# Kernel optimization log

Hardware: AMD Instinct MI355X
Metric: run time of the kernel (lower is better)

## Reference

```python
import jax, jax.numpy as jnp
import numpy as np

B, D, H, W, C = 8, 24, 24, 24, 192
NH = 6
WS = (4, 4, 4)
SS = (2, 2, 2)
HIDDEN = 4 * C
CPB_H = 512


def _buffers():
    wd, wh, ww = WS
    rd = np.arange(-(wd - 1), wd, dtype=np.float32)
    rh = np.arange(-(wh - 1), wh, dtype=np.float32)
    rw = np.arange(-(ww - 1), ww, dtype=np.float32)
    table = np.stack(np.meshgrid(rd, rh, rw, indexing='ij'), axis=-1)[None]  # (1,2wd-1,2wh-1,2ww-1,3)
    table[..., 0] /= (wd - 1)
    table[..., 1] /= (wh - 1)
    table[..., 2] /= (ww - 1)
    table *= 8.0
    table = np.sign(table) * np.log2(np.abs(table) + 1.0) / np.log2(8.0)
    coords = np.stack(np.meshgrid(np.arange(wd), np.arange(wh), np.arange(ww), indexing='ij'))
    cf = coords.reshape(3, -1)
    rel = (cf[:, :, None] - cf[:, None, :]).transpose(1, 2, 0).astype(np.int64)
    rel[..., 0] += wd - 1
    rel[..., 1] += wh - 1
    rel[..., 2] += ww - 1
    rel[..., 0] *= (2 * wh - 1) * (2 * ww - 1)
    rel[..., 1] *= (2 * ww - 1)
    return table.astype(np.float32), rel.sum(-1).astype(np.int32)


def _attn_mask():
    wd, wh, ww = WS
    img = np.zeros((1, D, H, W, 1), np.float32)
    cnt = 0
    def sl(w, s):
        return (slice(0, -w), slice(-w, -s), slice(-s, None))
    for d_ in sl(wd, SS[0]):
        for h_ in sl(wh, SS[1]):
            for w_ in sl(ww, SS[2]):
                img[:, d_, h_, w_, :] = cnt
                cnt += 1
    mw = img.reshape(1, D // wd, wd, H // wh, wh, W // ww, ww, 1)
    mw = mw.transpose(0, 1, 3, 5, 2, 4, 6, 7).reshape(-1, wd * wh * ww)  # (nW, N)
    am = mw[:, None, :] - mw[:, :, None]
    return np.where(am != 0, -100.0, 0.0).astype(np.float32)


def setup_inputs() -> dict:
    key = jax.random.key(0)
    ks = jax.random.split(key, 8)
    w = lambda k, shape: jax.random.normal(k, shape, jnp.float32) * 0.02
    table, rpi = _buffers()
    return {
        'x': jax.random.normal(ks[0], (B, D, H, W, C), jnp.float32),
        'norm1_w': jnp.ones((C,), jnp.float32), 'norm1_b': jnp.zeros((C,), jnp.float32),
        'qkv_w': w(ks[1], (3 * C, C)),
        'q_bias': jnp.zeros((C,), jnp.float32), 'v_bias': jnp.zeros((C,), jnp.float32),
        'logit_scale': jnp.log(10.0) * jnp.ones((NH, 1, 1), jnp.float32),
        'cpb_w1': w(ks[2], (CPB_H, 3)), 'cpb_b1': jnp.zeros((CPB_H,), jnp.float32),
        'cpb_w2': w(ks[3], (NH, CPB_H)),
        'proj_w': w(ks[4], (C, C)), 'proj_b': jnp.zeros((C,), jnp.float32),
        'norm2_w': jnp.ones((C,), jnp.float32), 'norm2_b': jnp.zeros((C,), jnp.float32),
        'fc1_w': w(ks[5], (HIDDEN, C)), 'fc1_b': jnp.zeros((HIDDEN,), jnp.float32),
        'fc2_w': w(ks[6], (C, HIDDEN)), 'fc2_b': jnp.zeros((C,), jnp.float32),
        'rel_table': jnp.asarray(table),
        'rel_index': jnp.asarray(rpi),
        'attn_mask': jnp.asarray(_attn_mask()),
    }


def _ln(x, w, b):
    mu = x.mean(-1, keepdims=True)
    var = ((x - mu) ** 2).mean(-1, keepdims=True)
    return (x - mu) * jax.lax.rsqrt(var + 1e-5) * w + b


def _forward(x, norm1_w, norm1_b, qkv_w, q_bias, v_bias, logit_scale,
             cpb_w1, cpb_b1, cpb_w2, proj_w, proj_b, norm2_w, norm2_b,
             fc1_w, fc1_b, fc2_w, fc2_b, rel_table, rel_index, attn_mask):
    wd, wh, ww = WS
    N = wd * wh * ww
    hd = C // NH
    shortcut = x
    h = _ln(x, norm1_w, norm1_b)
    h = jnp.roll(h, (-SS[0], -SS[1], -SS[2]), axis=(1, 2, 3))
    # window partition -> (B*nW, N, C)
    xw = h.reshape(B, D // wd, wd, H // wh, wh, W // ww, ww, C)
    xw = xw.transpose(0, 1, 3, 5, 2, 4, 6, 7).reshape(-1, N, C)
    B_ = xw.shape[0]
    # NOTE: faithful to torch source, where qkv is recomputed via self.qkv(x)
    # (bias=False), discarding the assembled qkv_bias. q_bias/v_bias thus unused.
    qkv = (xw @ qkv_w.T).reshape(B_, N, 3, NH, hd).transpose(2, 0, 3, 1, 4)
    q, k, v = qkv[0], qkv[1], qkv[2]  # each (B_, NH, N, hd)
    qn = q / jnp.maximum(jnp.linalg.norm(q, axis=-1, keepdims=True), 1e-12)
    kn = k / jnp.maximum(jnp.linalg.norm(k, axis=-1, keepdims=True), 1e-12)
    attn = jnp.einsum('bhnd,bhmd->bhnm', qn, kn)
    scale = jnp.exp(jnp.minimum(logit_scale, jnp.log(100.0)))  # (NH,1,1)
    attn = attn * scale
    # continuous position bias MLP -> gather per relative index
    bias_table = jax.nn.relu(rel_table.reshape(-1, 3) @ cpb_w1.T + cpb_b1) @ cpb_w2.T  # (T, NH)
    rpb = bias_table[rel_index.reshape(-1)].reshape(N, N, NH).transpose(2, 0, 1)
    attn = attn + 16.0 * jax.nn.sigmoid(rpb)[None]
    nW = attn_mask.shape[0]
    attn = attn.reshape(B_ // nW, nW, NH, N, N) + attn_mask[None, :, None]
    attn = jax.nn.softmax(attn.reshape(B_, NH, N, N), axis=-1)
    out = jnp.einsum('bhnm,bhmd->bhnd', attn, v).transpose(0, 2, 1, 3).reshape(B_, N, C)
    out = out @ proj_w.T + proj_b
    # window reverse -> (B, D, H, W, C)
    out = out.reshape(B, D // wd, H // wh, W // ww, wd, wh, ww, C)
    out = out.transpose(0, 1, 4, 2, 5, 3, 6, 7).reshape(B, D, H, W, C)
    out = jnp.roll(out, (SS[0], SS[1], SS[2]), axis=(1, 2, 3))
    h = shortcut + out
    m = _ln(h, norm2_w, norm2_b)
    m = jax.nn.gelu(m @ fc1_w.T + fc1_b, approximate=False)
    m = m @ fc2_w.T + fc2_b
    return h + m


def reference(x, norm1_w, norm1_b, qkv_w, q_bias, v_bias, logit_scale,
              cpb_w1, cpb_b1, cpb_w2, proj_w, proj_b, norm2_w, norm2_b,
              fc1_w, fc1_b, fc2_w, fc2_b, rel_table, rel_index, attn_mask):
    return _forward(x, norm1_w, norm1_b, qkv_w, q_bias, v_bias, logit_scale,
                    cpb_w1, cpb_b1, cpb_w2, proj_w, proj_b, norm2_w, norm2_b,
                    fc1_w, fc1_b, fc2_w, fc2_b, rel_table, rel_index, attn_mask)
```

## Files before the change

### kernel.cpp

```cpp
#include <hip/hip_runtime.h>
#include <hip/hip_bf16.h>
#include <math.h>

typedef __attribute__((ext_vector_type(8))) short bf16x8;
typedef __attribute__((ext_vector_type(4))) float f32x4;

__device__ inline ushort f2bf(float f) {
    __hip_bfloat16 h = __float2bfloat16(f);
    return *reinterpret_cast<ushort*>(&h);
}
__device__ inline float bf2f(ushort u) {
    return __uint_as_float(((unsigned int)u) << 16);
}

__global__ __launch_bounds__(256) void k_cpb_table(
        const float* __restrict__ rtab, const float* __restrict__ w1,
        const float* __restrict__ b1, const float* __restrict__ w2,
        float* __restrict__ table_out) {
    int idx = blockIdx.x * 256 + threadIdx.x;
    if (idx >= 343 * 6) return;
    int r = idx / 6, head = idx - r * 6;
    float t0 = rtab[r*3+0], t1 = rtab[r*3+1], t2 = rtab[r*3+2];
    float s = 0.f;
    for (int j = 0; j < 512; ++j) {
        float a = t0*w1[j*3+0] + t1*w1[j*3+1] + t2*w1[j*3+2] + b1[j];
        a = fmaxf(a, 0.f);
        s += a * w2[head*512 + j];
    }
    table_out[idx] = s;
}

__global__ __launch_bounds__(256) void k_bias16(
        const float* __restrict__ table_out, const int* __restrict__ ridx,
        float* __restrict__ bias16) {
    int idx = blockIdx.x * 256 + threadIdx.x;
    if (idx >= 6 * 64 * 64) return;
    int head = idx >> 12;
    int nm = idx & 4095;
    float v = table_out[ridx[nm] * 6 + head];
    bias16[idx] = 16.f / (1.f + expf(-v));
}

__global__ __launch_bounds__(256) void k_wcvt(
        const float* __restrict__ qkvw, const float* __restrict__ f1w,
        const float* __restrict__ f2w, const float* __restrict__ pw,
        ushort* __restrict__ Wqb, ushort* __restrict__ W1b,
        ushort* __restrict__ W2b, ushort* __restrict__ Wpb) {
    int i = blockIdx.x * 256 + threadIdx.x;
    W1b[i] = f2bf(f1w[i]);
    W2b[i] = f2bf(f2w[i]);
    if (i < 110592) Wqb[i] = f2bf(qkvw[i]);
    if (i < 36864)  Wpb[i] = f2bf(pw[i]);
}

__global__ __launch_bounds__(256) void k_ln1(
        const float* __restrict__ x, const float* __restrict__ nw,
        const float* __restrict__ nb, ushort* __restrict__ buf1) {
    const int wb = blockIdx.x;
    const int b = wb / 216, win = wb - b * 216;
    const int wdi = win / 36, whi = (win / 6) % 6, wwi = win % 6;
    const int t = threadIdx.x;
    const int n = t >> 2, sub = t & 3;
    const int id = n >> 4, ih = (n >> 2) & 3, iw = n & 3;
    const int dsrc = (wdi*4 + id + 2) % 24;
    const int hsrc = (whi*4 + ih + 2) % 24;
    const int wsrc = (wwi*4 + iw + 2) % 24;
    const float* xr = x + (size_t)(((b*24 + dsrc)*24 + hsrc)*24 + wsrc) * 192 + sub*48;
    float4 q[12];
    float sum = 0.f, ssum = 0.f;
    #pragma unroll
    for (int j = 0; j < 12; ++j) {
        q[j] = reinterpret_cast<const float4*>(xr)[j];
        sum  += q[j].x + q[j].y + q[j].z + q[j].w;
        ssum += q[j].x*q[j].x + q[j].y*q[j].y + q[j].z*q[j].z + q[j].w*q[j].w;
    }
    sum  += __shfl_xor(sum, 1);  sum  += __shfl_xor(sum, 2);
    ssum += __shfl_xor(ssum, 1); ssum += __shfl_xor(ssum, 2);
    float mu = sum * (1.f/192.f);
    float inv = rsqrtf(ssum * (1.f/192.f) - mu*mu + 1e-5f);
    ushort* op = buf1 + ((size_t)wb*64 + n)*192 + sub*48;
    #pragma unroll
    for (int j = 0; j < 12; ++j) {
        int c = sub*48 + j*4;
        ushort4 o;
        o.x = f2bf((q[j].x - mu)*inv*nw[c+0] + nb[c+0]);
        o.y = f2bf((q[j].y - mu)*inv*nw[c+1] + nb[c+1]);
        o.z = f2bf((q[j].z - mu)*inv*nw[c+2] + nb[c+2]);
        o.w = f2bf((q[j].w - mu)*inv*nw[c+3] + nb[c+3]);
        *reinterpret_cast<ushort4*>(op + j*4) = o;
    }
}

__global__ __launch_bounds__(256) void k_attn3(
        const ushort* __restrict__ buf1, const ushort* __restrict__ Wqb,
        const float* __restrict__ ls, const float* __restrict__ bias16,
        const float* __restrict__ amask, ushort* __restrict__ buf2) {
    __shared__ ushort QK[2][3][64][40];
    __shared__ ushort Vt[3][32][72];
    __shared__ ushort Pl[4][16][72];
    const int wb = blockIdx.x;
    const int win = wb % 216;
    const int t = threadIdx.x;
    const int wid = t >> 6, lane = t & 63;
    const int fr = lane & 15, fg = lane >> 4;
    const int trow = wid * 16;
    const ushort* Abase = buf1 + (size_t)wb * 12288 + (size_t)(trow + fr) * 192 + fg * 8;

    for (int g = 0; g < 2; ++g) {
        if (g) __syncthreads();
        f32x4 acc[18] = {};
        #pragma unroll
        for (int ks = 0; ks < 6; ++ks) {
            bf16x8 a = *(const bf16x8*)(Abase + ks*32);
            #pragma unroll
            for (int ct = 0; ct < 18; ++ct) {
                const int seg = ct / 6, u = ct % 6;
                const int gcol = seg*192 + g*96 + u*16;
                bf16x8 b = *(const bf16x8*)(Wqb + (size_t)(gcol + fr)*192 + ks*32 + fg*8);
                acc[ct] = __builtin_amdgcn_mfma_f32_16x16x32_bf16(a, b, acc[ct], 0, 0, 0);
            }
        }
        #pragma unroll
        for (int ct = 0; ct < 18; ++ct) {
            const int seg = ct / 6, u = ct % 6;
            const int hl = u >> 1, dp = u & 1;
            if (seg < 2) {
                #pragma unroll
                for (int e = 0; e < 4; ++e)
                    QK[seg][hl][trow + fg*4 + e][dp*16 + fr] = f2bf(acc[ct][e]);
            } else {
                ushort4 v4;
                v4.x = f2bf(acc[ct][0]); v4.y = f2bf(acc[ct][1]);
                v4.z = f2bf(acc[ct][2]); v4.w = f2bf(acc[ct][3]);
                *reinterpret_cast<ushort4*>(&Vt[hl][dp*16 + fr][trow + fg*4]) = v4;
            }
        }
        __syncthreads();
        {
            float scq[3];
            #pragma unroll
            for (int hl = 0; hl < 3; ++hl)
                scq[hl] = expf(fminf(ls[g*3 + hl], 4.6051701859880914f));
            for (int rr = t; rr < 384; rr += 256) {
                const int mat = rr / 192, rem = rr - mat*192;
                const int hl = rem >> 6, n = rem & 63;
                ushort* p = &QK[mat][hl][n][0];
                float vals[32];
                float ss = 0.f;
                #pragma unroll
                for (int j = 0; j < 8; ++j) {
                    ushort4 u4 = *reinterpret_cast<const ushort4*>(p + j*4);
                    float a0 = bf2f(u4.x), a1 = bf2f(u4.y), a2 = bf2f(u4.z), a3 = bf2f(u4.w);
                    vals[j*4+0]=a0; vals[j*4+1]=a1; vals[j*4+2]=a2; vals[j*4+3]=a3;
                    ss += a0*a0 + a1*a1 + a2*a2 + a3*a3;
                }
                float f = 1.f / fmaxf(sqrtf(ss), 1e-12f);
                if (mat == 0) f *= (hl == 0 ? scq[0] : (hl == 1 ? scq[1] : scq[2]));
                #pragma unroll
                for (int j = 0; j < 8; ++j) {
                    ushort4 o;
                    o.x = f2bf(vals[j*4+0]*f); o.y = f2bf(vals[j*4+1]*f);
                    o.z = f2bf(vals[j*4+2]*f); o.w = f2bf(vals[j*4+3]*f);
                    *reinterpret_cast<ushort4*>(p + j*4) = o;
                }
            }
        }
        __syncthreads();
        #pragma unroll 1
        for (int hl = 0; hl < 3; ++hl) {
            const int h = g*3 + hl;
            bf16x8 qf = *(const bf16x8*)&QK[0][hl][trow + fr][fg*8];
            f32x4 accS[4] = {};
            #pragma unroll
            for (int j = 0; j < 4; ++j) {
                bf16x8 kf = *(const bf16x8*)&QK[1][hl][j*16 + fr][fg*8];
                accS[j] = __builtin_amdgcn_mfma_f32_16x16x32_bf16(qf, kf, accS[j], 0, 0, 0);
            }
            float s[4][4];
            const float* bi = bias16 + h*4096;
            const float* mk = amask + (size_t)win*4096;
            #pragma unroll
            for (int e = 0; e < 4; ++e) {
                const int r = trow + fg*4 + e;
                #pragma unroll
                for (int j = 0; j < 4; ++j) {
                    const int c = j*16 + fr;
                    s[j][e] = accS[j][e] + bi[r*64 + c] + mk[r*64 + c];
                }
            }
            #pragma unroll
            for (int e = 0; e < 4; ++e) {
                float m0 = fmaxf(fmaxf(s[0][e], s[1][e]), fmaxf(s[2][e], s[3][e]));
                m0 = fmaxf(m0, __shfl_xor(m0, 1));
                m0 = fmaxf(m0, __shfl_xor(m0, 2));
                m0 = fmaxf(m0, __shfl_xor(m0, 4));
                m0 = fmaxf(m0, __shfl_xor(m0, 8));
                float s0 = 0.f;
                #pragma unroll
                for (int j = 0; j < 4; ++j) { s[j][e] = expf(s[j][e] - m0); s0 += s[j][e]; }
                s0 += __shfl_xor(s0, 1);
                s0 += __shfl_xor(s0, 2);
                s0 += __shfl_xor(s0, 4);
                s0 += __shfl_xor(s0, 8);
                const float rs = 1.f / s0;
                #pragma unroll
                for (int j = 0; j < 4; ++j)
                    Pl[wid][fg*4 + e][j*16 + fr] = f2bf(s[j][e] * rs);
            }
            f32x4 accO[2] = {};
            #pragma unroll
            for (int kk = 0; kk < 2; ++kk) {
                bf16x8 pa = *(const bf16x8*)&Pl[wid][fr][kk*32 + fg*8];
                #pragma unroll
                for (int j = 0; j < 2; ++j) {
                    bf16x8 vb = *(const bf16x8*)&Vt[hl][j*16 + fr][kk*32 + fg*8];
                    accO[j] = __builtin_amdgcn_mfma_f32_16x16x32_bf16(pa, vb, accO[j], 0, 0, 0);
                }
            }
            #pragma unroll
            for (int j = 0; j < 2; ++j) {
                #pragma unroll
                for (int e = 0; e < 4; ++e) {
                    buf2[(size_t)wb*12288 + (size_t)(trow + fg*4 + e)*192 + h*32 + j*16 + fr]
                        = f2bf(accO[j][e]);
                }
            }
        }
    }
}

__global__ __launch_bounds__(256) void k_proj(
        const ushort* __restrict__ buf2, const float* __restrict__ x,
        const ushort* __restrict__ Wpb, const float* __restrict__ pb,
        float* __restrict__ out) {
    __shared__ ushort As[64 * 200];
    __shared__ int rowbase[64];
    const int t = threadIdx.x;
    const size_t base = (size_t)blockIdx.x * 64;
    if (t < 64) {
        int dst = (int)base + t;
        int b = dst / 13824, r1 = dst - b * 13824;
        int d = r1 / 576, h2 = (r1 / 24) % 24, w2 = r1 % 24;
        int dd = (d + 22) % 24, hh = (h2 + 22) % 24, ww = (w2 + 22) % 24;
        int win = ((dd >> 2)*6 + (hh >> 2))*6 + (ww >> 2);
        int n = ((dd & 3) << 4) | ((hh & 3) << 2) | (ww & 3);
        rowbase[t] = ((b*216 + win)*64 + n) * 192;
    }
    __syncthreads();
    {
        const int r = t >> 2, q = t & 3;
        const ushort* src = buf2 + rowbase[r] + q*48;
        #pragma unroll
        for (int i = 0; i < 6; ++i)
            *(bf16x8*)(As + r*200 + q*48 + i*8) = *(const bf16x8*)(src + i*8);
    }
    __syncthreads();

    const int wid = t >> 6, lane = t & 63;
    const int fr = lane & 15, fg = lane >> 4;
    const int trow = wid * 16;
    f32x4 acc[12] = {};
    #pragma unroll
    for (int ks = 0; ks < 6; ++ks) {
        bf16x8 a = *(const bf16x8*)(As + (trow + fr)*200 + ks*32 + fg*8);
        #pragma unroll
        for (int j = 0; j < 12; ++j) {
            bf16x8 b = *(const bf16x8*)(Wpb + (size_t)(j*16 + fr)*192 + ks*32 + fg*8);
            acc[j] = __builtin_amdgcn_mfma_f32_16x16x32_bf16(a, b, acc[j], 0, 0, 0);
        }
    }
    #pragma unroll
    for (int j = 0; j < 12; ++j) {
        int c = j*16 + fr;
        float bias = pb[c];
        #pragma unroll
        for (int e = 0; e < 4; ++e) {
            size_t idx = (base + trow + fg*4 + e)*192 + c;
            out[idx] = x[idx] + acc[j][e] + bias;
        }
    }
}

__global__ __launch_bounds__(256) void k_mlp2(
        const ushort* __restrict__ W1b, const ushort* __restrict__ W2b,
        const float* __restrict__ n2w, const float* __restrict__ n2b,
        const float* __restrict__ f1b, const float* __restrict__ f2b,
        float* __restrict__ out) {
    __shared__ ushort As[64 * 200];
    __shared__ ushort Hs[64 * 136];
    const int t = threadIdx.x;
    const size_t tok0 = (size_t)blockIdx.x * 64;

    {
        const int r = t >> 2, q = t & 3;
        const float* hp = out + (tok0 + r) * 192 + q * 48;
        float4 v[12];
        float sum = 0.f, ssum = 0.f;
        #pragma unroll
        for (int j = 0; j < 12; ++j) {
            v[j] = reinterpret_cast<const float4*>(hp)[j];
            sum  += v[j].x + v[j].y + v[j].z + v[j].w;
            ssum += v[j].x*v[j].x + v[j].y*v[j].y + v[j].z*v[j].z + v[j].w*v[j].w;
        }
        sum  += __shfl_xor(sum, 1);  sum  += __shfl_xor(sum, 2);
        ssum += __shfl_xor(ssum, 1); ssum += __shfl_xor(ssum, 2);
        float mu = sum * (1.f/192.f);
        float inv = rsqrtf(ssum * (1.f/192.f) - mu*mu + 1e-5f);
        #pragma unroll
        for (int j = 0; j < 12; ++j) {
            int c = q*48 + j*4;
            ushort4 o;
            o.x = f2bf((v[j].x - mu)*inv*n2w[c+0] + n2b[c+0]);
            o.y = f2bf((v[j].y - mu)*inv*n2w[c+1] + n2b[c+1]);
            o.z = f2bf((v[j].z - mu)*inv*n2w[c+2] + n2b[c+2]);
            o.w = f2bf((v[j].w - mu)*inv*n2w[c+3] + n2b[c+3]);
            *reinterpret_cast<ushort4*>(As + r*200 + c) = o;
        }
    }
    __syncthreads();

    const int wid = t >> 6, lane = t & 63;
    const int fr = lane & 15, fg = lane >> 4;
    const int trow = wid * 16;
    f32x4 acc2[12] = {};

    for (int hb = 0; hb < 768; hb += 128) {
        f32x4 acc1[8] = {};
        #pragma unroll
        for (int ks = 0; ks < 6; ++ks) {
            bf16x8 a = *(const bf16x8*)(As + (trow + fr)*200 + ks*32 + fg*8);
            #pragma unroll
            for (int j = 0; j < 8; ++j) {
                bf16x8 b = *(const bf16x8*)(W1b + (size_t)(hb + j*16 + fr)*192 + ks*32 + fg*8);
                acc1[j] = __builtin_amdgcn_mfma_f32_16x16x32_bf16(a, b, acc1[j], 0, 0, 0);
            }
        }
        __syncthreads();
        #pragma unroll
        for (int j = 0; j < 8; ++j) {
            float bias = f1b[hb + j*16 + fr];
            #pragma unroll
            for (int e = 0; e < 4; ++e) {
                float h = acc1[j][e] + bias;
                h = 0.5f*h*(1.f + erff(h*0.70710678118654752f));
                Hs[(trow + fg*4 + e)*136 + j*16 + fr] = f2bf(h);
            }
        }
        __syncthreads();
        #pragma unroll
        for (int ks = 0; ks < 4; ++ks) {
            bf16x8 a = *(const bf16x8*)(Hs + (trow + fr)*136 + ks*32 + fg*8);
            #pragma unroll
            for (int j = 0; j < 12; ++j) {
                bf16x8 b = *(const bf16x8*)(W2b + (size_t)(j*16 + fr)*768 + hb + ks*32 + fg*8);
                acc2[j] = __builtin_amdgcn_mfma_f32_16x16x32_bf16(a, b, acc2[j], 0, 0, 0);
            }
        }
    }

    #pragma unroll
    for (int j = 0; j < 12; ++j) {
        int c = j*16 + fr;
        float bias = f2b[c];
        #pragma unroll
        for (int e = 0; e < 4; ++e) {
            size_t idx = (tok0 + trow + fg*4 + e)*192 + c;
            out[idx] += acc2[j][e] + bias;
        }
    }
}

extern "C" void kernel_launch(void* const* d_in, const int* in_sizes, int n_in,
                              void* d_out, int out_size, void* d_ws, size_t ws_size,
                              hipStream_t stream) {
    const float* x     = (const float*)d_in[0];
    const float* n1w   = (const float*)d_in[1];
    const float* n1b   = (const float*)d_in[2];
    const float* qkvw  = (const float*)d_in[3];
    const float* ls    = (const float*)d_in[6];
    const float* cpw1  = (const float*)d_in[7];
    const float* cpb1  = (const float*)d_in[8];
    const float* cpw2  = (const float*)d_in[9];
    const float* pw    = (const float*)d_in[10];
    const float* pb    = (const float*)d_in[11];
    const float* n2w   = (const float*)d_in[12];
    const float* n2b   = (const float*)d_in[13];
    const float* f1w   = (const float*)d_in[14];
    const float* f1b   = (const float*)d_in[15];
    const float* f2w   = (const float*)d_in[16];
    const float* f2b   = (const float*)d_in[17];
    const float* rtab  = (const float*)d_in[18];
    const int*   ridx  = (const int*)d_in[19];
    const float* amask = (const float*)d_in[20];
    float* out = (float*)d_out;

    ushort* buf1 = (ushort*)d_ws;
    ushort* buf2 = buf1 + 21233664;
    ushort* Wqb  = buf2 + 21233664;
    ushort* W1b  = Wqb + 110592;
    ushort* W2b  = W1b + 147456;
    ushort* Wpb  = W2b + 147456;
    float*  tblo = (float*)(Wpb + 36864);
    float*  b16  = tblo + 2064;

    k_cpb_table<<<dim3(9),    dim3(256), 0, stream>>>(rtab, cpw1, cpb1, cpw2, tblo);
    k_bias16   <<<dim3(96),   dim3(256), 0, stream>>>(tblo, ridx, b16);
    k_wcvt     <<<dim3(576),  dim3(256), 0, stream>>>(qkvw, f1w, f2w, pw, Wqb, W1b, W2b, Wpb);
    k_ln1      <<<dim3(1728), dim3(256), 0, stream>>>(x, n1w, n1b, buf1);
    k_attn3    <<<dim3(1728), dim3(256), 0, stream>>>(buf1, Wqb, ls, b16, amask, buf2);
    k_proj     <<<dim3(1728), dim3(256), 0, stream>>>(buf2, x, Wpb, pb, out);
    k_mlp2     <<<dim3(1728), dim3(256), 0, stream>>>(W1b, W2b, n2w, n2b, f1b, f2b, out);
}
```

Baseline: 1.150 ms.

## Give each wave 32 tokens in MLP kernel to reuse weight fragments

The MLP kernel now assigns 32 tokens per wave (128 per block) instead of 16, so every W1/W2 fragment loaded from global memory feeds two MFMAs. This halves weight traffic per token. LayerNorm output and the GELU hidden tile become per-wave private, which removes the block-wide __syncthreads. The A fragments are held in registers across the hidden loop, and the hidden chunk shrinks to 64. The risk is higher register pressure (acc2 grows to 24 f32x4 plus 12 A fragments) under launch_bounds(256,2), and the grid is halved.

```diff
diff --git a/kernel.cpp b/kernel.cpp
--- a/kernel.cpp
+++ b/kernel.cpp
@@ -281,79 +281,90 @@
     }
 }
 
-__global__ __launch_bounds__(256) void k_mlp2(
+__global__ __launch_bounds__(256, 2) void k_mlp3(
         const ushort* __restrict__ W1b, const ushort* __restrict__ W2b,
         const float* __restrict__ n2w, const float* __restrict__ n2b,
         const float* __restrict__ f1b, const float* __restrict__ f2b,
         float* __restrict__ out) {
-    __shared__ ushort As[64 * 200];
-    __shared__ ushort Hs[64 * 136];
+    __shared__ ushort As[4][32][200];
+    __shared__ ushort Hs[4][32][68];
     const int t = threadIdx.x;
-    const size_t tok0 = (size_t)blockIdx.x * 64;
+    const int wid = t >> 6, lane = t & 63;
+    const size_t tok0 = (size_t)blockIdx.x * 128 + wid * 32;
 
     {
-        const int r = t >> 2, q = t & 3;
-        const float* hp = out + (tok0 + r) * 192 + q * 48;
-        float4 v[12];
+        const int r = lane >> 1, half = lane & 1;
+        const float* hp = out + (tok0 + r) * 192 + half * 96;
+        float4 v[24];
         float sum = 0.f, ssum = 0.f;
         #pragma unroll
-        for (int j = 0; j < 12; ++j) {
+        for (int j = 0; j < 24; ++j) {
             v[j] = reinterpret_cast<const float4*>(hp)[j];
             sum  += v[j].x + v[j].y + v[j].z + v[j].w;
             ssum += v[j].x*v[j].x + v[j].y*v[j].y + v[j].z*v[j].z + v[j].w*v[j].w;
         }
-        sum  += __shfl_xor(sum, 1);  sum  += __shfl_xor(sum, 2);
-        ssum += __shfl_xor(ssum, 1); ssum += __shfl_xor(ssum, 2);
+        sum  += __shfl_xor(sum, 1);
+        ssum += __shfl_xor(ssum, 1);
         float mu = sum * (1.f/192.f);
         float inv = rsqrtf(ssum * (1.f/192.f) - mu*mu + 1e-5f);
         #pragma unroll
-        for (int j = 0; j < 12; ++j) {
-            int c = q*48 + j*4;
+        for (int j = 0; j < 24; ++j) {
+            int c = half*96 + j*4;
             ushort4 o;
             o.x = f2bf((v[j].x - mu)*inv*n2w[c+0] + n2b[c+0]);
             o.y = f2bf((v[j].y - mu)*inv*n2w[c+1] + n2b[c+1]);
             o.z = f2bf((v[j].z - mu)*inv*n2w[c+2] + n2b[c+2]);
             o.w = f2bf((v[j].w - mu)*inv*n2w[c+3] + n2b[c+3]);
-            *reinterpret_cast<ushort4*>(As + r*200 + c) = o;
-        }
-    }
-    __syncthreads();
-
-    const int wid = t >> 6, lane = t & 63;
+            *reinterpret_cast<ushort4*>(&As[wid][r][c]) = o;
+        }
+    }
+
     const int fr = lane & 15, fg = lane >> 4;
-    const int trow = wid * 16;
-    f32x4 acc2[12] = {};
-
-    for (int hb = 0; hb < 768; hb += 128) {
-        f32x4 acc1[8] = {};
+    bf16x8 a[2][6];
+    #pragma unroll
+    for (int tf = 0; tf < 2; ++tf)
+        #pragma unroll
+        for (int ks = 0; ks < 6; ++ks)
+            a[tf][ks] = *(const bf16x8*)&As[wid][tf*16 + fr][ks*32 + fg*8];
+
+    f32x4 acc2[2][12] = {};
+
+    for (int hb = 0; hb < 768; hb += 64) {
+        f32x4 acc1[2][4] = {};
         #pragma unroll
         for (int ks = 0; ks < 6; ++ks) {
-            bf16x8 a = *(const bf16x8*)(As + (trow + fr)*200 + ks*32 + fg*8);
-            #pragma unroll
-            for (int j = 0; j < 8; ++j) {
-                bf16x8 b = *(const bf16x8*)(W1b + (size_t)(hb + j*16 + fr)*192 + ks*32 + fg*8);
-                acc1[j] = __builtin_amdgcn_mfma_f32_16x16x32_bf16(a, b, acc1[j], 0, 0, 0);
-            }
-        }
-        __syncthreads();
-        #pragma unroll
-        for (int j = 0; j < 8; ++j) {
+            bf16x8 b[4];
+            #pragma unroll
+            for (int j = 0; j < 4; ++j)
+                b[j] = *(const bf16x8*)(W1b + (size_t)(hb + j*16 + fr)*192 + ks*32 + fg*8);
+            #pragma unroll
+            for (int j = 0; j < 4; ++j) {
+                acc1[0][j] = __builtin_amdgcn_mfma_f32_16x16x32_bf16(a[0][ks], b[j], acc1[0][j], 0, 0, 0);
+                acc1[1][j] = __builtin_amdgcn_mfma_f32_16x16x32_bf16(a[1][ks], b[j], acc1[1][j], 0, 0, 0);
+            }
+        }
+        #pragma unroll
+        for (int j = 0; j < 4; ++j) {
             float bias = f1b[hb + j*16 + fr];
             #pragma unroll
-            for (int e = 0; e < 4; ++e) {
-                float h = acc1[j][e] + bias;
-                h = 0.5f*h*(1.f + erff(h*0.70710678118654752f));
-                Hs[(trow + fg*4 + e)*136 + j*16 + fr] = f2bf(h);
-            }
-        }
-        __syncthreads();
-        #pragma unroll
-        for (int ks = 0; ks < 4; ++ks) {
-            bf16x8 a = *(const bf16x8*)(Hs + (trow + fr)*136 + ks*32 + fg*8);
+            for (int tf = 0; tf < 2; ++tf) {
+                #pragma unroll
+                for (int e = 0; e < 4; ++e) {
+                    float h = acc1[tf][j][e] + bias;
+                    h = 0.5f*h*(1.f + erff(h*0.70710678118654752f));
+                    Hs[wid][tf*16 + fg*4 + e][j*16 + fr] = f2bf(h);
+                }
+            }
+        }
+        #pragma unroll
+        for (int ks2 = 0; ks2 < 2; ++ks2) {
+            bf16x8 ha0 = *(const bf16x8*)&Hs[wid][fr][ks2*32 + fg*8];
+            bf16x8 ha1 = *(const bf16x8*)&Hs[wid][16 + fr][ks2*32 + fg*8];
             #pragma unroll
             for (int j = 0; j < 12; ++j) {
-                bf16x8 b = *(const bf16x8*)(W2b + (size_t)(j*16 + fr)*768 + hb + ks*32 + fg*8);
-                acc2[j] = __builtin_amdgcn_mfma_f32_16x16x32_bf16(a, b, acc2[j], 0, 0, 0);
+                bf16x8 b = *(const bf16x8*)(W2b + (size_t)(j*16 + fr)*768 + hb + ks2*32 + fg*8);
+                acc2[0][j] = __builtin_amdgcn_mfma_f32_16x16x32_bf16(ha0, b, acc2[0][j], 0, 0, 0);
+                acc2[1][j] = __builtin_amdgcn_mfma_f32_16x16x32_bf16(ha1, b, acc2[1][j], 0, 0, 0);
             }
         }
     }
@@ -363,9 +374,12 @@
         int c = j*16 + fr;
         float bias = f2b[c];
         #pragma unroll
-        for (int e = 0; e < 4; ++e) {
-            size_t idx = (tok0 + trow + fg*4 + e)*192 + c;
-            out[idx] += acc2[j][e] + bias;
+        for (int tf = 0; tf < 2; ++tf) {
+            #pragma unroll
+            for (int e = 0; e < 4; ++e) {
+                size_t idx = (tok0 + tf*16 + fg*4 + e)*192 + c;
+                out[idx] += acc2[tf][j][e] + bias;
+            }
         }
     }
 }
@@ -409,5 +423,5 @@
     k_ln1      <<<dim3(1728), dim3(256), 0, stream>>>(x, n1w, n1b, buf1);
     k_attn3    <<<dim3(1728), dim3(256), 0, stream>>>(buf1, Wqb, ls, b16, amask, buf2);
     k_proj     <<<dim3(1728), dim3(256), 0, stream>>>(buf2, x, Wpb, pb, out);
-    k_mlp2     <<<dim3(1728), dim3(256), 0, stream>>>(W1b, W2b, n2w, n2b, f1b, f2b, out);
-}
+    k_mlp3     <<<dim3(864),  dim3(256), 0, stream>>>(W1b, W2b, n2w, n2b, f1b, f2b, out);
+}
```

After: 966.7 us. 16.0% less time.
